# Kernel optimization log

Measured on AMD Instinct MI355X. Metric: run time of the kernel, lower is better.

The kernel has to match this reference:

```python
import jax, jax.numpy as jnp
import numpy as np

MEMORY_SIZE = 8192
FEATURE_DIM = 512
NUM_QUERIES = 32768
EPS = 1e-12  # guard for sqrt in cdist


def setup_inputs() -> dict:
    key = jax.random.key(0)
    k1, k2, k3, k4 = jax.random.split(key, 4)
    return {
        "features": jax.random.normal(k1, (MEMORY_SIZE, FEATURE_DIM), dtype=jnp.float32),
        "positions": jax.random.normal(k2, (MEMORY_SIZE, 3), dtype=jnp.float32),
        "query_positions": jax.random.normal(k3, (NUM_QUERIES, 3), dtype=jnp.float32),
        "position_embeddings": jax.random.normal(k4, (MEMORY_SIZE, 3), dtype=jnp.float32),
    }


def _cdist(a, b):
    # Euclidean distance via ||a||^2 + ||b||^2 - 2 a.b; avoids [Q,M,3] intermediate.
    a2 = jnp.sum(a * a, axis=-1, keepdims=True)          # [Q,1]
    b2 = jnp.sum(b * b, axis=-1, keepdims=True).T        # [1,M]
    d2 = a2 + b2 - 2.0 * (a @ b.T)                       # [Q,M]
    return jnp.sqrt(jnp.maximum(d2, EPS))


def reference(features, positions, query_positions, position_embeddings):
    # --- update ---
    positions_norm = positions / jnp.linalg.norm(positions, axis=-1, keepdims=True)
    embeddings_norm = position_embeddings / jnp.linalg.norm(position_embeddings, axis=-1, keepdims=True)
    sim = positions_norm @ embeddings_norm.T             # [M,M]
    attn = jax.nn.softmax(sim, axis=-1)
    memory = attn @ features                              # [M,F]
    new_pos_emb = attn @ positions                        # [M,3]
    # --- query ---
    dist = _cdist(query_positions, new_pos_emb)           # [Q,M]
    qattn = jax.nn.softmax(-dist, axis=-1)
    retrieved = qattn @ memory                            # [Q,F]
    return retrieved
```

## Files before the change

kernel.cpp:

```cpp
#include <hip/hip_runtime.h>
#include <stdint.h>
#include <stddef.h>

#define M_SZ 8192
#define F_DIM 512
#define N_Q 32768

typedef __attribute__((ext_vector_type(4))) float f32x4;
typedef __attribute__((ext_vector_type(8))) __bf16 bf16x8;
typedef __attribute__((ext_vector_type(2))) __bf16 bf16x2;

__device__ __forceinline__ float bits_to_f(unsigned u) {
    union { unsigned u; float f; } v; v.u = u; return v.f;
}
__device__ __forceinline__ unsigned pk_bf16(float a, float b) {
    union { bf16x2 v; unsigned u; } cv;
    cv.v.x = (__bf16)a; cv.v.y = (__bf16)b;
    return cv.u;
}
__device__ __forceinline__ unsigned short f2bf(float x) {
    union { bf16x2 v; unsigned u; } cv;
    cv.v.x = (__bf16)x; cv.v.y = (__bf16)0.0f;
    return (unsigned short)(cv.u & 0xffffu);
}
__device__ __forceinline__ bf16x8 as_bf16x8(uint4 u) {
    union { uint4 a; bf16x8 b; } cv; cv.a = u; return cv.b;
}

__global__ void prep_kernel(const float* __restrict__ pos,
                            const float* __restrict__ emb,
                            float* __restrict__ pn4,
                            float* __restrict__ en4,
                            float* __restrict__ pos4) {
    int i = blockIdx.x * 256 + threadIdx.x;
    if (i >= M_SZ) return;
    float x = pos[i * 3 + 0], y = pos[i * 3 + 1], z = pos[i * 3 + 2];
    float inv = 1.0f / __builtin_amdgcn_sqrtf(x * x + y * y + z * z);
    pn4[i * 4 + 0] = x * inv; pn4[i * 4 + 1] = y * inv;
    pn4[i * 4 + 2] = z * inv; pn4[i * 4 + 3] = 0.0f;
    pos4[i * 4 + 0] = x; pos4[i * 4 + 1] = y;
    pos4[i * 4 + 2] = z; pos4[i * 4 + 3] = 0.0f;
    float ex = emb[i * 3 + 0], ey = emb[i * 3 + 1], ez = emb[i * 3 + 2];
    float einv = 1.0f / __builtin_amdgcn_sqrtf(ex * ex + ey * ey + ez * ez);
    en4[i * 4 + 0] = ex * einv; en4[i * 4 + 1] = ey * einv;
    en4[i * 4 + 2] = ez * einv; en4[i * 4 + 3] = 0.0f;
}

__global__ void transpose_kernel(const float* __restrict__ feat,
                                 unsigned short* __restrict__ featT) {
    __shared__ float tile[64 * 65];
    const int jb = blockIdx.x * 64, fb = blockIdx.y * 64;
    const int t = threadIdx.x;
#pragma unroll
    for (int p = 0; p < 16; ++p) {
        int idx = p * 256 + t;
        int j = idx >> 6, f = idx & 63;
        tile[j * 65 + f] = feat[(size_t)(jb + j) * F_DIM + fb + f];
    }
    __syncthreads();
#pragma unroll
    for (int p = 0; p < 16; ++p) {
        int idx = p * 256 + t;
        int f = idx >> 6, j = idx & 63;
        featT[(size_t)(fb + f) * M_SZ + jb + j] = f2bf(tile[j * 65 + f]);
    }
}

__launch_bounds__(512, 2)
__global__ void build_memory_kernel(const float* __restrict__ pn4,
                                    const float* __restrict__ en4,
                                    const float* __restrict__ pos4,
                                    const unsigned short* __restrict__ featT,
                                    unsigned short* __restrict__ memT,
                                    float* __restrict__ npe4) {
    constexpr int BM = 32, BK = 32, PSTR = BK + 8;
    __shared__ unsigned short pbuf[2][BM * PSTR];
    __shared__ f32x4 red4[512];
    __shared__ float lbuf[BM];

    const int t = threadIdx.x;
    const int lane = t & 63, wv = t >> 6;
    const int col = lane & 15, quad = lane >> 4;
    const int mb = blockIdx.x * BM;
    const int r = t & 31, jq = t >> 5;

    const f32x4 pnr = ((const f32x4*)pn4)[mb + r];
    const f32x4* en = (const f32x4*)en4;
    const f32x4* ps = (const f32x4*)pos4;

    const unsigned short* bp[4];
#pragma unroll
    for (int n = 0; n < 4; ++n)
        bp[n] = featT + (size_t)(wv * 64 + n * 16 + col) * M_SZ + quad * 8;

    f32x4 acc[2][4];
    const f32x4 zero4 = {0.f, 0.f, 0.f, 0.f};
#pragma unroll
    for (int m = 0; m < 2; ++m)
#pragma unroll
        for (int n = 0; n < 4; ++n) acc[m][n] = zero4;
    float nx = 0.f, ny = 0.f, nz = 0.f, lp = 0.f;

    uint4 vbA[4], vbB[4];
#pragma unroll
    for (int n = 0; n < 4; ++n) vbA[n] = *(const uint4*)(bp[n]);

#define B_GEN_P(JB, SIDE)                                                    \
    {                                                                        \
        int j = (JB) + jq * 2;                                               \
        f32x4 e0 = en[j], e1 = en[j + 1];                                    \
        f32x4 p0 = ps[j], p1 = ps[j + 1];                                    \
        float s0 = fmaf(pnr.x, e0.x, fmaf(pnr.y, e0.y, pnr.z * e0.z));       \
        float s1 = fmaf(pnr.x, e1.x, fmaf(pnr.y, e1.y, pnr.z * e1.z));       \
        float w0 = __builtin_amdgcn_exp2f(s0 * 1.44269504f);                 \
        float w1 = __builtin_amdgcn_exp2f(s1 * 1.44269504f);                 \
        unsigned u = pk_bf16(w0, w1);                                        \
        float w0r = bits_to_f(u << 16), w1r = bits_to_f(u & 0xffff0000u);    \
        lp += w0r + w1r;                                                     \
        nx = fmaf(w0r, p0.x, fmaf(w1r, p1.x, nx));                           \
        ny = fmaf(w0r, p0.y, fmaf(w1r, p1.y, ny));                           \
        nz = fmaf(w0r, p0.z, fmaf(w1r, p1.z, nz));                           \
        *(unsigned*)(&pbuf[SIDE][r * PSTR + jq * 2]) = u;                    \
    }

#define B_MFMA(VB, SIDE)                                                     \
    {                                                                        \
        _Pragma("unroll") for (int m = 0; m < 2; ++m) {                      \
            bf16x8 a = *(const bf16x8*)(&pbuf[SIDE][(m * 16 + col) * PSTR + quad * 8]); \
            _Pragma("unroll") for (int n = 0; n < 4; ++n)                    \
                acc[m][n] = __builtin_amdgcn_mfma_f32_16x16x32_bf16(         \
                    a, as_bf16x8(VB[n]), acc[m][n], 0, 0, 0);                \
        }                                                                    \
    }

#define B_BODY(CUR, NXT, SIDE, JNXT)                                         \
    {                                                                        \
        _Pragma("unroll") for (int n = 0; n < 4; ++n) {                      \
            NXT[n] = *(const uint4*)(bp[n] + BK);                            \
            bp[n] += BK;                                                     \
        }                                                                    \
        B_GEN_P(JNXT, SIDE ^ 1)                                              \
        B_MFMA(CUR, SIDE)                                                    \
        __syncthreads();                                                     \
    }

    B_GEN_P(0, 0)
    __syncthreads();

    int jn = BK;
    for (int kt = 0; kt < 254; kt += 2) {
        B_BODY(vbA, vbB, 0, jn) jn += BK;
        B_BODY(vbB, vbA, 1, jn) jn += BK;
    }
    B_BODY(vbA, vbB, 0, jn)
    B_MFMA(vbB, 1)
#undef B_BODY
#undef B_MFMA
#undef B_GEN_P

    f32x4 mine = {nx, ny, nz, lp};
    red4[t] = mine;
    __syncthreads();
    if (t < BM) {
        f32x4 s = red4[t];
#pragma unroll
        for (int g = 1; g < 16; ++g) {
            f32x4 o = red4[t + 32 * g];
            s.x += o.x; s.y += o.y; s.z += o.z; s.w += o.w;
        }
        lbuf[t] = s.w;
        float inv = 1.0f / s.w;
        float X = s.x * inv, Y = s.y * inv, Z = s.z * inv;
        f32x4 o = {X, Y, Z, X * X + Y * Y + Z * Z};
        ((f32x4*)npe4)[mb + t] = o;
    }
    __syncthreads();

#pragma unroll
    for (int m = 0; m < 2; ++m) {
        f32x4 l4 = *(const f32x4*)(lbuf + m * 16 + quad * 4);
        f32x4 inv4 = {1.0f / l4.x, 1.0f / l4.y, 1.0f / l4.z, 1.0f / l4.w};
        int mg = mb + m * 16 + quad * 4;
#pragma unroll
        for (int n = 0; n < 4; ++n) {
            int fg = wv * 64 + n * 16 + col;
            uint2 o;
            o.x = pk_bf16(acc[m][n].x * inv4.x, acc[m][n].y * inv4.y);
            o.y = pk_bf16(acc[m][n].z * inv4.z, acc[m][n].w * inv4.w);
            *(uint2*)(memT + (size_t)fg * M_SZ + mg) = o;
        }
    }
}

__launch_bounds__(512, 2)
__global__ void query_kernel(const float* __restrict__ qpos,
                             const float* __restrict__ npe4,
                             const unsigned short* __restrict__ memT,
                             float* __restrict__ out) {
    constexpr int BM = 128, BK = 32, PSTR = BK + 8;
    __shared__ unsigned short pbuf[2][BM * PSTR];
    __shared__ float redl[512];
    __shared__ float lbuf[BM];

    const int t = threadIdx.x;
    const int lane = t & 63, wv = t >> 6;
    const int col = lane & 15, quad = lane >> 4;
    const int qb = blockIdx.x * BM;
    const int r = t & 127, jq = t >> 7;

    const float qx = qpos[(size_t)(qb + r) * 3 + 0];
    const float qy = qpos[(size_t)(qb + r) * 3 + 1];
    const float qz = qpos[(size_t)(qb + r) * 3 + 2];
    const float q2 = qx * qx + qy * qy + qz * qz;
    const float m2x = -2.0f * qx, m2y = -2.0f * qy, m2z = -2.0f * qz;

    const f32x4* nsrc = (const f32x4*)npe4;

    const unsigned short* bp[4];
#pragma unroll
    for (int n = 0; n < 4; ++n)
        bp[n] = memT + (size_t)(wv * 64 + n * 16 + col) * M_SZ + quad * 8;

    f32x4 acc[8][4];
    const f32x4 zero4 = {0.f, 0.f, 0.f, 0.f};
#pragma unroll
    for (int m = 0; m < 8; ++m)
#pragma unroll
        for (int n = 0; n < 4; ++n) acc[m][n] = zero4;
    float lp = 0.f;

    uint4 vbA[4], vbB[4];
#pragma unroll
    for (int n = 0; n < 4; ++n) vbA[n] = *(const uint4*)(bp[n]);

#define Q_GEN_P(JB, SIDE)                                                    \
    {                                                                        \
        unsigned pk4[4];                                                     \
        _Pragma("unroll") for (int i = 0; i < 8; i += 2) {                   \
            int j = (JB) + jq * 8 + i;                                       \
            f32x4 n0 = nsrc[j], n1 = nsrc[j + 1];                            \
            float s0 = fmaf(m2x, n0.x, fmaf(m2y, n0.y, fmaf(m2z, n0.z, q2 + n0.w))); \
            float s1 = fmaf(m2x, n1.x, fmaf(m2y, n1.y, fmaf(m2z, n1.z, q2 + n1.w))); \
            s0 = fmaxf(s0, 1e-12f); s1 = fmaxf(s1, 1e-12f);                  \
            float w0 = __builtin_amdgcn_exp2f(__builtin_amdgcn_sqrtf(s0) * -1.44269504f); \
            float w1 = __builtin_amdgcn_exp2f(__builtin_amdgcn_sqrtf(s1) * -1.44269504f); \
            unsigned u = pk_bf16(w0, w1);                                    \
            lp += bits_to_f(u << 16) + bits_to_f(u & 0xffff0000u);           \
            pk4[i >> 1] = u;                                                 \
        }                                                                    \
        *(uint4*)(&pbuf[SIDE][r * PSTR + jq * 8]) =                          \
            make_uint4(pk4[0], pk4[1], pk4[2], pk4[3]);                      \
    }

#define Q_MFMA(VB, SIDE)                                                     \
    {                                                                        \
        _Pragma("unroll") for (int m = 0; m < 8; ++m) {                      \
            bf16x8 a = *(const bf16x8*)(&pbuf[SIDE][(m * 16 + col) * PSTR + quad * 8]); \
            _Pragma("unroll") for (int n = 0; n < 4; ++n)                    \
                acc[m][n] = __builtin_amdgcn_mfma_f32_16x16x32_bf16(         \
                    a, as_bf16x8(VB[n]), acc[m][n], 0, 0, 0);                \
        }                                                                    \
    }

#define Q_BODY(CUR, NXT, SIDE, JNXT)                                         \
    {                                                                        \
        _Pragma("unroll") for (int n = 0; n < 4; ++n) {                      \
            NXT[n] = *(const uint4*)(bp[n] + BK);                            \
            bp[n] += BK;                                                     \
        }                                                                    \
        Q_GEN_P(JNXT, SIDE ^ 1)                                              \
        Q_MFMA(CUR, SIDE)                                                    \
        __syncthreads();                                                     \
    }

    Q_GEN_P(0, 0)
    __syncthreads();

    int jn = BK;
    for (int kt = 0; kt < 254; kt += 2) {
        Q_BODY(vbA, vbB, 0, jn) jn += BK;
        Q_BODY(vbB, vbA, 1, jn) jn += BK;
    }
    Q_BODY(vbA, vbB, 0, jn)
    Q_MFMA(vbB, 1)
#undef Q_BODY
#undef Q_MFMA
#undef Q_GEN_P

    redl[t] = lp;
    __syncthreads();
    if (t < BM) lbuf[t] = redl[t] + redl[t + 128] + redl[t + 256] + redl[t + 384];
    __syncthreads();

#pragma unroll
    for (int m = 0; m < 8; ++m) {
        f32x4 l4 = *(const f32x4*)(lbuf + m * 16 + quad * 4);
        f32x4 inv4 = {1.0f / l4.x, 1.0f / l4.y, 1.0f / l4.z, 1.0f / l4.w};
        int qg = qb + m * 16 + quad * 4;
#pragma unroll
        for (int n = 0; n < 4; ++n) {
            int fg = wv * 64 + n * 16 + col;
            out[(size_t)(qg + 0) * F_DIM + fg] = acc[m][n].x * inv4.x;
            out[(size_t)(qg + 1) * F_DIM + fg] = acc[m][n].y * inv4.y;
            out[(size_t)(qg + 2) * F_DIM + fg] = acc[m][n].z * inv4.z;
            out[(size_t)(qg + 3) * F_DIM + fg] = acc[m][n].w * inv4.w;
        }
    }
}

extern "C" void kernel_launch(void* const* d_in, const int* in_sizes, int n_in,
                              void* d_out, int out_size, void* d_ws, size_t ws_size,
                              hipStream_t stream) {
    const float* features  = (const float*)d_in[0];
    const float* positions = (const float*)d_in[1];
    const float* qpos      = (const float*)d_in[2];
    const float* pemb      = (const float*)d_in[3];
    float* out = (float*)d_out;
    char* ws = (char*)d_ws;

    unsigned short* featT = (unsigned short*)(ws);
    unsigned short* memT  = (unsigned short*)(ws + 8388608);
    float* npe4 = (float*)(ws + 16777216);
    float* pn4  = (float*)(ws + 16908288);
    float* en4  = (float*)(ws + 17039360);
    float* pos4 = (float*)(ws + 17170432);

    hipLaunchKernelGGL(prep_kernel, dim3(M_SZ / 256), dim3(256), 0, stream,
                       positions, pemb, pn4, en4, pos4);
    hipLaunchKernelGGL(transpose_kernel, dim3(M_SZ / 64, F_DIM / 64), dim3(256), 0, stream,
                       features, featT);
    hipLaunchKernelGGL(build_memory_kernel, dim3(M_SZ / 32), dim3(512), 0, stream,
                       pn4, en4, pos4, featT, memT, npe4);
    hipLaunchKernelGGL(query_kernel, dim3(N_Q / 128), dim3(512), 0, stream,
                       qpos, npe4, memT, out);
}
```

Baseline: 815.3 us.

## Deepen K-tiles in build kernel and split query kernel across feature halves

```diff
diff --git a/kernel.cpp b/kernel.cpp
--- a/kernel.cpp
+++ b/kernel.cpp
@@ -73,7 +73,7 @@
                                     const unsigned short* __restrict__ featT,
                                     unsigned short* __restrict__ memT,
                                     float* __restrict__ npe4) {
-    constexpr int BM = 32, BK = 32, PSTR = BK + 8;
+    constexpr int BM = 32, BK = 128, PSTR = BK + 8;
     __shared__ unsigned short pbuf[2][BM * PSTR];
     __shared__ f32x4 red4[512];
     __shared__ float lbuf[BM];
@@ -101,44 +101,55 @@
         for (int n = 0; n < 4; ++n) acc[m][n] = zero4;
     float nx = 0.f, ny = 0.f, nz = 0.f, lp = 0.f;
 
-    uint4 vbA[4], vbB[4];
-#pragma unroll
-    for (int n = 0; n < 4; ++n) vbA[n] = *(const uint4*)(bp[n]);
+    uint4 vbA[4][4], vbB[4][4];
+#pragma unroll
+    for (int ks = 0; ks < 4; ++ks)
+#pragma unroll
+        for (int n = 0; n < 4; ++n)
+            vbA[ks][n] = *(const uint4*)(bp[n] + ks * 32);
 
 #define B_GEN_P(JB, SIDE)                                                    \
     {                                                                        \
-        int j = (JB) + jq * 2;                                               \
-        f32x4 e0 = en[j], e1 = en[j + 1];                                    \
-        f32x4 p0 = ps[j], p1 = ps[j + 1];                                    \
-        float s0 = fmaf(pnr.x, e0.x, fmaf(pnr.y, e0.y, pnr.z * e0.z));       \
-        float s1 = fmaf(pnr.x, e1.x, fmaf(pnr.y, e1.y, pnr.z * e1.z));       \
-        float w0 = __builtin_amdgcn_exp2f(s0 * 1.44269504f);                 \
-        float w1 = __builtin_amdgcn_exp2f(s1 * 1.44269504f);                 \
-        unsigned u = pk_bf16(w0, w1);                                        \
-        float w0r = bits_to_f(u << 16), w1r = bits_to_f(u & 0xffff0000u);    \
-        lp += w0r + w1r;                                                     \
-        nx = fmaf(w0r, p0.x, fmaf(w1r, p1.x, nx));                           \
-        ny = fmaf(w0r, p0.y, fmaf(w1r, p1.y, ny));                           \
-        nz = fmaf(w0r, p0.z, fmaf(w1r, p1.z, nz));                           \
-        *(unsigned*)(&pbuf[SIDE][r * PSTR + jq * 2]) = u;                    \
+        unsigned pk4[4];                                                     \
+        _Pragma("unroll") for (int i = 0; i < 8; i += 2) {                   \
+            int j = (JB) + jq * 8 + i;                                       \
+            f32x4 e0 = en[j], e1 = en[j + 1];                                \
+            f32x4 p0 = ps[j], p1 = ps[j + 1];                                \
+            float s0 = fmaf(pnr.x, e0.x, fmaf(pnr.y, e0.y, pnr.z * e0.z));   \
+            float s1 = fmaf(pnr.x, e1.x, fmaf(pnr.y, e1.y, pnr.z * e1.z));   \
+            float w0 = __builtin_amdgcn_exp2f(s0 * 1.44269504f);             \
+            float w1 = __builtin_amdgcn_exp2f(s1 * 1.44269504f);             \
+            unsigned u = pk_bf16(w0, w1);                                    \
+            float w0r = bits_to_f(u << 16), w1r = bits_to_f(u & 0xffff0000u);\
+            lp += w0r + w1r;                                                 \
+            nx = fmaf(w0r, p0.x, fmaf(w1r, p1.x, nx));                       \
+            ny = fmaf(w0r, p0.y, fmaf(w1r, p1.y, ny));                       \
+            nz = fmaf(w0r, p0.z, fmaf(w1r, p1.z, nz));                       \
+            pk4[i >> 1] = u;                                                 \
+        }                                                                    \
+        *(uint4*)(&pbuf[SIDE][r * PSTR + jq * 8]) =                          \
+            make_uint4(pk4[0], pk4[1], pk4[2], pk4[3]);                      \
     }
 
 #define B_MFMA(VB, SIDE)                                                     \
     {                                                                        \
-        _Pragma("unroll") for (int m = 0; m < 2; ++m) {                      \
-            bf16x8 a = *(const bf16x8*)(&pbuf[SIDE][(m * 16 + col) * PSTR + quad * 8]); \
+        _Pragma("unroll") for (int ks = 0; ks < 4; ++ks) {                   \
+            _Pragma("unroll") for (int m = 0; m < 2; ++m) {                  \
+                bf16x8 a = *(const bf16x8*)(                                 \
+                    &pbuf[SIDE][(m * 16 + col) * PSTR + ks * 32 + quad * 8]);\
+                _Pragma("unroll") for (int n = 0; n < 4; ++n)                \
+                    acc[m][n] = __builtin_amdgcn_mfma_f32_16x16x32_bf16(     \
+                        a, as_bf16x8(VB[ks][n]), acc[m][n], 0, 0, 0);        \
+            }                                                                \
+        }                                                                    \
+    }
+
+#define B_BODY(CUR, NXT, SIDE, JNXT)                                         \
+    {                                                                        \
+        _Pragma("unroll") for (int ks = 0; ks < 4; ++ks)                     \
             _Pragma("unroll") for (int n = 0; n < 4; ++n)                    \
-                acc[m][n] = __builtin_amdgcn_mfma_f32_16x16x32_bf16(         \
-                    a, as_bf16x8(VB[n]), acc[m][n], 0, 0, 0);                \
-        }                                                                    \
-    }
-
-#define B_BODY(CUR, NXT, SIDE, JNXT)                                         \
-    {                                                                        \
-        _Pragma("unroll") for (int n = 0; n < 4; ++n) {                      \
-            NXT[n] = *(const uint4*)(bp[n] + BK);                            \
-            bp[n] += BK;                                                     \
-        }                                                                    \
+                NXT[ks][n] = *(const uint4*)(bp[n] + BK + ks * 32);          \
+        _Pragma("unroll") for (int n = 0; n < 4; ++n) bp[n] += BK;           \
         B_GEN_P(JNXT, SIDE ^ 1)                                              \
         B_MFMA(CUR, SIDE)                                                    \
         __syncthreads();                                                     \
@@ -148,7 +159,7 @@
     __syncthreads();
 
     int jn = BK;
-    for (int kt = 0; kt < 254; kt += 2) {
+    for (int kt = 0; kt < 62; kt += 2) {
         B_BODY(vbA, vbB, 0, jn) jn += BK;
         B_BODY(vbB, vbA, 1, jn) jn += BK;
     }
@@ -192,21 +203,21 @@
     }
 }
 
-__launch_bounds__(512, 2)
+__launch_bounds__(256, 2)
 __global__ void query_kernel(const float* __restrict__ qpos,
                              const float* __restrict__ npe4,
                              const unsigned short* __restrict__ memT,
                              float* __restrict__ out) {
-    constexpr int BM = 128, BK = 32, PSTR = BK + 8;
+    constexpr int BM = 64, BK = 64, PSTR = BK + 8;
     __shared__ unsigned short pbuf[2][BM * PSTR];
-    __shared__ float redl[512];
+    __shared__ float redl[256];
     __shared__ float lbuf[BM];
 
     const int t = threadIdx.x;
     const int lane = t & 63, wv = t >> 6;
     const int col = lane & 15, quad = lane >> 4;
-    const int qb = blockIdx.x * BM;
-    const int r = t & 127, jq = t >> 7;
+    const int qb = blockIdx.x * BM, fb = blockIdx.y * 256;
+    const int r = t & 63, jq = t >> 6;
 
     const float qx = qpos[(size_t)(qb + r) * 3 + 0];
     const float qy = qpos[(size_t)(qb + r) * 3 + 1];
@@ -219,25 +230,28 @@
     const unsigned short* bp[4];
 #pragma unroll
     for (int n = 0; n < 4; ++n)
-        bp[n] = memT + (size_t)(wv * 64 + n * 16 + col) * M_SZ + quad * 8;
-
-    f32x4 acc[8][4];
+        bp[n] = memT + (size_t)(fb + wv * 64 + n * 16 + col) * M_SZ + quad * 8;
+
+    f32x4 acc[4][4];
     const f32x4 zero4 = {0.f, 0.f, 0.f, 0.f};
 #pragma unroll
-    for (int m = 0; m < 8; ++m)
+    for (int m = 0; m < 4; ++m)
 #pragma unroll
         for (int n = 0; n < 4; ++n) acc[m][n] = zero4;
     float lp = 0.f;
 
-    uint4 vbA[4], vbB[4];
-#pragma unroll
-    for (int n = 0; n < 4; ++n) vbA[n] = *(const uint4*)(bp[n]);
+    uint4 vbA[2][4], vbB[2][4];
+#pragma unroll
+    for (int ks = 0; ks < 2; ++ks)
+#pragma unroll
+        for (int n = 0; n < 4; ++n)
+            vbA[ks][n] = *(const uint4*)(bp[n] + ks * 32);
 
 #define Q_GEN_P(JB, SIDE)                                                    \
     {                                                                        \
-        unsigned pk4[4];                                                     \
-        _Pragma("unroll") for (int i = 0; i < 8; i += 2) {                   \
-            int j = (JB) + jq * 8 + i;                                       \
+        unsigned pk8[8];                                                     \
+        _Pragma("unroll") for (int i = 0; i < 16; i += 2) {                  \
+            int j = (JB) + jq * 16 + i;                                      \
             f32x4 n0 = nsrc[j], n1 = nsrc[j + 1];                            \
             float s0 = fmaf(m2x, n0.x, fmaf(m2y, n0.y, fmaf(m2z, n0.z, q2 + n0.w))); \
             float s1 = fmaf(m2x, n1.x, fmaf(m2y, n1.y, fmaf(m2z, n1.z, q2 + n1.w))); \
@@ -246,28 +260,32 @@
             float w1 = __builtin_amdgcn_exp2f(__builtin_amdgcn_sqrtf(s1) * -1.44269504f); \
             unsigned u = pk_bf16(w0, w1);                                    \
             lp += bits_to_f(u << 16) + bits_to_f(u & 0xffff0000u);           \
-            pk4[i >> 1] = u;                                                 \
+            pk8[i >> 1] = u;                                                 \
         }                                                                    \
-        *(uint4*)(&pbuf[SIDE][r * PSTR + jq * 8]) =                          \
-            make_uint4(pk4[0], pk4[1], pk4[2], pk4[3]);                      \
+        uint4* pd = (uint4*)(&pbuf[SIDE][r * PSTR + jq * 16]);               \
+        pd[0] = make_uint4(pk8[0], pk8[1], pk8[2], pk8[3]);                  \
+        pd[1] = make_uint4(pk8[4], pk8[5], pk8[6], pk8[7]);                  \
     }
 
 #define Q_MFMA(VB, SIDE)                                                     \
     {                                                                        \
-        _Pragma("unroll") for (int m = 0; m < 8; ++m) {                      \
-            bf16x8 a = *(const bf16x8*)(&pbuf[SIDE][(m * 16 + col) * PSTR + quad * 8]); \
+        _Pragma("unroll") for (int ks = 0; ks < 2; ++ks) {                   \
+            _Pragma("unroll") for (int m = 0; m < 4; ++m) {                  \
+                bf16x8 a = *(const bf16x8*)(                                 \
+                    &pbuf[SIDE][(m * 16 + col) * PSTR + ks * 32 + quad * 8]);\
+                _Pragma("unroll") for (int n = 0; n < 4; ++n)                \
+                    acc[m][n] = __builtin_amdgcn_mfma_f32_16x16x32_bf16(     \
+                        a, as_bf16x8(VB[ks][n]), acc[m][n], 0, 0, 0);        \
+            }                                                                \
+        }                                                                    \
+    }
+
+#define Q_BODY(CUR, NXT, SIDE, JNXT)                                         \
+    {                                                                        \
+        _Pragma("unroll") for (int ks = 0; ks < 2; ++ks)                     \
             _Pragma("unroll") for (int n = 0; n < 4; ++n)                    \
-                acc[m][n] = __builtin_amdgcn_mfma_f32_16x16x32_bf16(         \
-                    a, as_bf16x8(VB[n]), acc[m][n], 0, 0, 0);                \
-        }                                                                    \
-    }
-
-#define Q_BODY(CUR, NXT, SIDE, JNXT)                                         \
-    {                                                                        \
-        _Pragma("unroll") for (int n = 0; n < 4; ++n) {                      \
-            NXT[n] = *(const uint4*)(bp[n] + BK);                            \
-            bp[n] += BK;                                                     \
-        }                                                                    \
+                NXT[ks][n] = *(const uint4*)(bp[n] + BK + ks * 32);          \
+        _Pragma("unroll") for (int n = 0; n < 4; ++n) bp[n] += BK;           \
         Q_GEN_P(JNXT, SIDE ^ 1)                                              \
         Q_MFMA(CUR, SIDE)                                                    \
         __syncthreads();                                                     \
@@ -277,7 +295,7 @@
     __syncthreads();
 
     int jn = BK;
-    for (int kt = 0; kt < 254; kt += 2) {
+    for (int kt = 0; kt < 126; kt += 2) {
         Q_BODY(vbA, vbB, 0, jn) jn += BK;
         Q_BODY(vbB, vbA, 1, jn) jn += BK;
     }
@@ -289,17 +307,17 @@
 
     redl[t] = lp;
     __syncthreads();
-    if (t < BM) lbuf[t] = redl[t] + redl[t + 128] + redl[t + 256] + redl[t + 384];
-    __syncthreads();
-
-#pragma unroll
-    for (int m = 0; m < 8; ++m) {
+    if (t < BM) lbuf[t] = redl[t] + redl[t + 64] + redl[t + 128] + redl[t + 192];
+    __syncthreads();
+
+#pragma unroll
+    for (int m = 0; m < 4; ++m) {
         f32x4 l4 = *(const f32x4*)(lbuf + m * 16 + quad * 4);
         f32x4 inv4 = {1.0f / l4.x, 1.0f / l4.y, 1.0f / l4.z, 1.0f / l4.w};
         int qg = qb + m * 16 + quad * 4;
 #pragma unroll
         for (int n = 0; n < 4; ++n) {
-            int fg = wv * 64 + n * 16 + col;
+            int fg = fb + wv * 64 + n * 16 + col;
             out[(size_t)(qg + 0) * F_DIM + fg] = acc[m][n].x * inv4.x;
             out[(size_t)(qg + 1) * F_DIM + fg] = acc[m][n].y * inv4.y;
             out[(size_t)(qg + 2) * F_DIM + fg] = acc[m][n].z * inv4.z;
@@ -331,6 +349,6 @@
                        features, featT);
     hipLaunchKernelGGL(build_memory_kernel, dim3(M_SZ / 32), dim3(512), 0, stream,
                        pn4, en4, pos4, featT, memT, npe4);
-    hipLaunchKernelGGL(query_kernel, dim3(N_Q / 128), dim3(512), 0, stream,
+    hipLaunchKernelGGL(query_kernel, dim3(N_Q / 64, 2), dim3(256), 0, stream,
                        qpos, npe4, memT, out);
 }
```

New measurement: 1.309 ms. +60.6%, slower.

## Shrink tiles and split feature dim to raise occupancy in build and query kernels

Applied to the files above, without the earlier changes.

```diff
diff --git a/kernel.cpp b/kernel.cpp
--- a/kernel.cpp
+++ b/kernel.cpp
@@ -66,32 +66,33 @@
     }
 }
 
-__launch_bounds__(512, 2)
+__launch_bounds__(256, 4)
 __global__ void build_memory_kernel(const float* __restrict__ pn4,
                                     const float* __restrict__ en4,
                                     const float* __restrict__ pos4,
                                     const unsigned short* __restrict__ featT,
                                     unsigned short* __restrict__ memT,
                                     float* __restrict__ npe4) {
-    constexpr int BM = 32, BK = 32, PSTR = BK + 8;
+    constexpr int BM = 32, BK = 32, PSTR = 40;
     __shared__ unsigned short pbuf[2][BM * PSTR];
-    __shared__ f32x4 red4[512];
+    __shared__ f32x4 red4[256];
     __shared__ float lbuf[BM];
 
     const int t = threadIdx.x;
     const int lane = t & 63, wv = t >> 6;
     const int col = lane & 15, quad = lane >> 4;
-    const int mb = blockIdx.x * BM;
+    const int mb = blockIdx.x * BM, fb = blockIdx.y * 256;
+    const bool y0 = (blockIdx.y == 0);
     const int r = t & 31, jq = t >> 5;
 
     const f32x4 pnr = ((const f32x4*)pn4)[mb + r];
     const f32x4* en = (const f32x4*)en4;
     const f32x4* ps = (const f32x4*)pos4;
 
-    const unsigned short* bp[4];
-#pragma unroll
-    for (int n = 0; n < 4; ++n)
-        bp[n] = featT + (size_t)(wv * 64 + n * 16 + col) * M_SZ + quad * 8;
+    const unsigned short* bp0 = featT + (size_t)(fb + wv * 64 + 0 + col) * M_SZ + quad * 8;
+    const unsigned short* bp1 = featT + (size_t)(fb + wv * 64 + 16 + col) * M_SZ + quad * 8;
+    const unsigned short* bp2 = featT + (size_t)(fb + wv * 64 + 32 + col) * M_SZ + quad * 8;
+    const unsigned short* bp3 = featT + (size_t)(fb + wv * 64 + 48 + col) * M_SZ + quad * 8;
 
     f32x4 acc[2][4];
     const f32x4 zero4 = {0.f, 0.f, 0.f, 0.f};
@@ -101,62 +102,59 @@
         for (int n = 0; n < 4; ++n) acc[m][n] = zero4;
     float nx = 0.f, ny = 0.f, nz = 0.f, lp = 0.f;
 
-    uint4 vbA[4], vbB[4];
-#pragma unroll
-    for (int n = 0; n < 4; ++n) vbA[n] = *(const uint4*)(bp[n]);
-
-#define B_GEN_P(JB, SIDE)                                                    \
+#define B_GEN(JB, SIDE)                                                      \
     {                                                                        \
-        int j = (JB) + jq * 2;                                               \
-        f32x4 e0 = en[j], e1 = en[j + 1];                                    \
-        f32x4 p0 = ps[j], p1 = ps[j + 1];                                    \
+        int j = (JB) + jq * 4;                                               \
+        f32x4 e0 = en[j], e1 = en[j + 1], e2 = en[j + 2], e3 = en[j + 3];    \
         float s0 = fmaf(pnr.x, e0.x, fmaf(pnr.y, e0.y, pnr.z * e0.z));       \
         float s1 = fmaf(pnr.x, e1.x, fmaf(pnr.y, e1.y, pnr.z * e1.z));       \
-        float w0 = __builtin_amdgcn_exp2f(s0 * 1.44269504f);                 \
-        float w1 = __builtin_amdgcn_exp2f(s1 * 1.44269504f);                 \
-        unsigned u = pk_bf16(w0, w1);                                        \
-        float w0r = bits_to_f(u << 16), w1r = bits_to_f(u & 0xffff0000u);    \
-        lp += w0r + w1r;                                                     \
-        nx = fmaf(w0r, p0.x, fmaf(w1r, p1.x, nx));                           \
-        ny = fmaf(w0r, p0.y, fmaf(w1r, p1.y, ny));                           \
-        nz = fmaf(w0r, p0.z, fmaf(w1r, p1.z, nz));                           \
-        *(unsigned*)(&pbuf[SIDE][r * PSTR + jq * 2]) = u;                    \
-    }
-
-#define B_MFMA(VB, SIDE)                                                     \
+        float s2 = fmaf(pnr.x, e2.x, fmaf(pnr.y, e2.y, pnr.z * e2.z));       \
+        float s3 = fmaf(pnr.x, e3.x, fmaf(pnr.y, e3.y, pnr.z * e3.z));       \
+        unsigned u0 = pk_bf16(__builtin_amdgcn_exp2f(s0 * 1.44269504f),      \
+                              __builtin_amdgcn_exp2f(s1 * 1.44269504f));     \
+        unsigned u1 = pk_bf16(__builtin_amdgcn_exp2f(s2 * 1.44269504f),      \
+                              __builtin_amdgcn_exp2f(s3 * 1.44269504f));     \
+        float w0 = bits_to_f(u0 << 16), w1 = bits_to_f(u0 & 0xffff0000u);    \
+        float w2 = bits_to_f(u1 << 16), w3 = bits_to_f(u1 & 0xffff0000u);    \
+        lp += (w0 + w1) + (w2 + w3);                                         \
+        if (y0) {                                                            \
+            f32x4 p0 = ps[j], p1 = ps[j + 1], p2 = ps[j + 2], p3 = ps[j + 3];\
+            nx += fmaf(w0, p0.x, w1 * p1.x) + fmaf(w2, p2.x, w3 * p3.x);     \
+            ny += fmaf(w0, p0.y, w1 * p1.y) + fmaf(w2, p2.y, w3 * p3.y);     \
+            nz += fmaf(w0, p0.z, w1 * p1.z) + fmaf(w2, p2.z, w3 * p3.z);     \
+        }                                                                    \
+        *(uint2*)(&pbuf[SIDE][r * PSTR + jq * 4]) = make_uint2(u0, u1);      \
+    }
+
+#define B_STEP(SIDE, DOGEN, DOSYNC, JB)                                      \
     {                                                                        \
+        uint4 vb0 = *(const uint4*)bp0; bp0 += BK;                           \
+        uint4 vb1 = *(const uint4*)bp1; bp1 += BK;                           \
+        uint4 vb2 = *(const uint4*)bp2; bp2 += BK;                           \
+        uint4 vb3 = *(const uint4*)bp3; bp3 += BK;                           \
+        if (DOGEN) B_GEN(JB, (SIDE) ^ 1)                                     \
         _Pragma("unroll") for (int m = 0; m < 2; ++m) {                      \
             bf16x8 a = *(const bf16x8*)(&pbuf[SIDE][(m * 16 + col) * PSTR + quad * 8]); \
-            _Pragma("unroll") for (int n = 0; n < 4; ++n)                    \
-                acc[m][n] = __builtin_amdgcn_mfma_f32_16x16x32_bf16(         \
-                    a, as_bf16x8(VB[n]), acc[m][n], 0, 0, 0);                \
+            acc[m][0] = __builtin_amdgcn_mfma_f32_16x16x32_bf16(a, as_bf16x8(vb0), acc[m][0], 0, 0, 0); \
+            acc[m][1] = __builtin_amdgcn_mfma_f32_16x16x32_bf16(a, as_bf16x8(vb1), acc[m][1], 0, 0, 0); \
+            acc[m][2] = __builtin_amdgcn_mfma_f32_16x16x32_bf16(a, as_bf16x8(vb2), acc[m][2], 0, 0, 0); \
+            acc[m][3] = __builtin_amdgcn_mfma_f32_16x16x32_bf16(a, as_bf16x8(vb3), acc[m][3], 0, 0, 0); \
         }                                                                    \
-    }
-
-#define B_BODY(CUR, NXT, SIDE, JNXT)                                         \
-    {                                                                        \
-        _Pragma("unroll") for (int n = 0; n < 4; ++n) {                      \
-            NXT[n] = *(const uint4*)(bp[n] + BK);                            \
-            bp[n] += BK;                                                     \
-        }                                                                    \
-        B_GEN_P(JNXT, SIDE ^ 1)                                              \
-        B_MFMA(CUR, SIDE)                                                    \
-        __syncthreads();                                                     \
-    }
-
-    B_GEN_P(0, 0)
+        if (DOSYNC) __syncthreads();                                         \
+    }
+
+    B_GEN(0, 0)
     __syncthreads();
 
     int jn = BK;
-    for (int kt = 0; kt < 254; kt += 2) {
-        B_BODY(vbA, vbB, 0, jn) jn += BK;
-        B_BODY(vbB, vbA, 1, jn) jn += BK;
-    }
-    B_BODY(vbA, vbB, 0, jn)
-    B_MFMA(vbB, 1)
-#undef B_BODY
-#undef B_MFMA
-#undef B_GEN_P
+    for (int i2 = 0; i2 < 127; ++i2) {
+        B_STEP(0, true, true, jn) jn += BK;
+        B_STEP(1, true, true, jn) jn += BK;
+    }
+    B_STEP(0, true, true, jn)
+    B_STEP(1, false, false, 0)
+#undef B_STEP
+#undef B_GEN
 
     f32x4 mine = {nx, ny, nz, lp};
     red4[t] = mine;
@@ -164,15 +162,17 @@
     if (t < BM) {
         f32x4 s = red4[t];
 #pragma unroll
-        for (int g = 1; g < 16; ++g) {
+        for (int g = 1; g < 8; ++g) {
             f32x4 o = red4[t + 32 * g];
             s.x += o.x; s.y += o.y; s.z += o.z; s.w += o.w;
         }
         lbuf[t] = s.w;
-        float inv = 1.0f / s.w;
-        float X = s.x * inv, Y = s.y * inv, Z = s.z * inv;
-        f32x4 o = {X, Y, Z, X * X + Y * Y + Z * Z};
-        ((f32x4*)npe4)[mb + t] = o;
+        if (y0) {
+            float inv = 1.0f / s.w;
+            float X = s.x * inv, Y = s.y * inv, Z = s.z * inv;
+            f32x4 o = {X, Y, Z, X * X + Y * Y + Z * Z};
+            ((f32x4*)npe4)[mb + t] = o;
+        }
     }
     __syncthreads();
 
@@ -183,7 +183,7 @@
         int mg = mb + m * 16 + quad * 4;
 #pragma unroll
         for (int n = 0; n < 4; ++n) {
-            int fg = wv * 64 + n * 16 + col;
+            int fg = fb + wv * 64 + n * 16 + col;
             uint2 o;
             o.x = pk_bf16(acc[m][n].x * inv4.x, acc[m][n].y * inv4.y);
             o.y = pk_bf16(acc[m][n].z * inv4.z, acc[m][n].w * inv4.w);
@@ -192,12 +192,12 @@
     }
 }
 
-__launch_bounds__(512, 2)
+__launch_bounds__(512, 4)
 __global__ void query_kernel(const float* __restrict__ qpos,
                              const float* __restrict__ npe4,
                              const unsigned short* __restrict__ memT,
                              float* __restrict__ out) {
-    constexpr int BM = 128, BK = 32, PSTR = BK + 8;
+    constexpr int BM = 64, BK = 32, PSTR = 40;
     __shared__ unsigned short pbuf[2][BM * PSTR];
     __shared__ float redl[512];
     __shared__ float lbuf[BM];
@@ -206,7 +206,7 @@
     const int lane = t & 63, wv = t >> 6;
     const int col = lane & 15, quad = lane >> 4;
     const int qb = blockIdx.x * BM;
-    const int r = t & 127, jq = t >> 7;
+    const int r = t & 63, jq = t >> 6;
 
     const float qx = qpos[(size_t)(qb + r) * 3 + 0];
     const float qy = qpos[(size_t)(qb + r) * 3 + 1];
@@ -216,84 +216,82 @@
 
     const f32x4* nsrc = (const f32x4*)npe4;
 
-    const unsigned short* bp[4];
-#pragma unroll
-    for (int n = 0; n < 4; ++n)
-        bp[n] = memT + (size_t)(wv * 64 + n * 16 + col) * M_SZ + quad * 8;
-
-    f32x4 acc[8][4];
+    const unsigned short* bp0 = memT + (size_t)(wv * 64 + 0 + col) * M_SZ + quad * 8;
+    const unsigned short* bp1 = memT + (size_t)(wv * 64 + 16 + col) * M_SZ + quad * 8;
+    const unsigned short* bp2 = memT + (size_t)(wv * 64 + 32 + col) * M_SZ + quad * 8;
+    const unsigned short* bp3 = memT + (size_t)(wv * 64 + 48 + col) * M_SZ + quad * 8;
+
+    f32x4 acc[4][4];
     const f32x4 zero4 = {0.f, 0.f, 0.f, 0.f};
 #pragma unroll
-    for (int m = 0; m < 8; ++m)
+    for (int m = 0; m < 4; ++m)
 #pragma unroll
         for (int n = 0; n < 4; ++n) acc[m][n] = zero4;
     float lp = 0.f;
 
-    uint4 vbA[4], vbB[4];
-#pragma unroll
-    for (int n = 0; n < 4; ++n) vbA[n] = *(const uint4*)(bp[n]);
-
-#define Q_GEN_P(JB, SIDE)                                                    \
+#define Q_GEN(JB, SIDE)                                                      \
     {                                                                        \
-        unsigned pk4[4];                                                     \
-        _Pragma("unroll") for (int i = 0; i < 8; i += 2) {                   \
-            int j = (JB) + jq * 8 + i;                                       \
-            f32x4 n0 = nsrc[j], n1 = nsrc[j + 1];                            \
-            float s0 = fmaf(m2x, n0.x, fmaf(m2y, n0.y, fmaf(m2z, n0.z, q2 + n0.w))); \
-            float s1 = fmaf(m2x, n1.x, fmaf(m2y, n1.y, fmaf(m2z, n1.z, q2 + n1.w))); \
-            s0 = fmaxf(s0, 1e-12f); s1 = fmaxf(s1, 1e-12f);                  \
-            float w0 = __builtin_amdgcn_exp2f(__builtin_amdgcn_sqrtf(s0) * -1.44269504f); \
-            float w1 = __builtin_amdgcn_exp2f(__builtin_amdgcn_sqrtf(s1) * -1.44269504f); \
-            unsigned u = pk_bf16(w0, w1);                                    \
-            lp += bits_to_f(u << 16) + bits_to_f(u & 0xffff0000u);           \
-            pk4[i >> 1] = u;                                                 \
+        int j = (JB) + jq * 4;                                               \
+        f32x4 n0 = nsrc[j], n1 = nsrc[j + 1], n2 = nsrc[j + 2], n3 = nsrc[j + 3]; \
+        float s0 = fmaf(m2x, n0.x, fmaf(m2y, n0.y, fmaf(m2z, n0.z, q2 + n0.w))); \
+        float s1 = fmaf(m2x, n1.x, fmaf(m2y, n1.y, fmaf(m2z, n1.z, q2 + n1.w))); \
+        float s2 = fmaf(m2x, n2.x, fmaf(m2y, n2.y, fmaf(m2z, n2.z, q2 + n2.w))); \
+        float s3 = fmaf(m2x, n3.x, fmaf(m2y, n3.y, fmaf(m2z, n3.z, q2 + n3.w))); \
+        s0 = fmaxf(s0, 1e-12f); s1 = fmaxf(s1, 1e-12f);                      \
+        s2 = fmaxf(s2, 1e-12f); s3 = fmaxf(s3, 1e-12f);                      \
+        float w0 = __builtin_amdgcn_exp2f(__builtin_amdgcn_sqrtf(s0) * -1.44269504f); \
+        float w1 = __builtin_amdgcn_exp2f(__builtin_amdgcn_sqrtf(s1) * -1.44269504f); \
+        float w2 = __builtin_amdgcn_exp2f(__builtin_amdgcn_sqrtf(s2) * -1.44269504f); \
+        float w3 = __builtin_amdgcn_exp2f(__builtin_amdgcn_sqrtf(s3) * -1.44269504f); \
+        unsigned u0 = pk_bf16(w0, w1);                                       \
+        unsigned u1 = pk_bf16(w2, w3);                                       \
+        lp += (bits_to_f(u0 << 16) + bits_to_f(u0 & 0xffff0000u)) +          \
+              (bits_to_f(u1 << 16) + bits_to_f(u1 & 0xffff0000u));           \
+        *(uint2*)(&pbuf[SIDE][r * PSTR + jq * 4]) = make_uint2(u0, u1);      \
+    }
+
+#define Q_STEP(SIDE, DOGEN, DOSYNC, JB)                                      \
+    {                                                                        \
+        uint4 vb0 = *(const uint4*)bp0; bp0 += BK;                           \
+        uint4 vb1 = *(const uint4*)bp1; bp1 += BK;                           \
+        uint4 vb2 = *(const uint4*)bp2; bp2 += BK;                           \
+        uint4 vb3 = *(const uint4*)bp3; bp3 += BK;                           \
+        if (DOGEN) Q_GEN(JB, (SIDE) ^ 1)                                     \
+        _Pragma("unroll") for (int m = 0; m < 4; ++m) {                      \
+            bf16x8 a = *(const bf16x8*)(&pbuf[SIDE][(m * 16 + col) * PSTR + quad * 8]); \
+            acc[m][0] = __builtin_amdgcn_mfma_f32_16x16x32_bf16(a, as_bf16x8(vb0), acc[m][0], 0, 0, 0); \
+            acc[m][1] = __builtin_amdgcn_mfma_f32_16x16x32_bf16(a, as_bf16x8(vb1), acc[m][1], 0, 0, 0); \
+            acc[m][2] = __builtin_amdgcn_mfma_f32_16x16x32_bf16(a, as_bf16x8(vb2), acc[m][2], 0, 0, 0); \
+            acc[m][3] = __builtin_amdgcn_mfma_f32_16x16x32_bf16(a, as_bf16x8(vb3), acc[m][3], 0, 0, 0); \
         }                                                                    \
-        *(uint4*)(&pbuf[SIDE][r * PSTR + jq * 8]) =                          \
-            make_uint4(pk4[0], pk4[1], pk4[2], pk4[3]);                      \
-    }
-
-#define Q_MFMA(VB, SIDE)                                                     \
-    {                                                                        \
-        _Pragma("unroll") for (int m = 0; m < 8; ++m) {                      \
-            bf16x8 a = *(const bf16x8*)(&pbuf[SIDE][(m * 16 + col) * PSTR + quad * 8]); \
-            _Pragma("unroll") for (int n = 0; n < 4; ++n)                    \
-                acc[m][n] = __builtin_amdgcn_mfma_f32_16x16x32_bf16(         \
-                    a, as_bf16x8(VB[n]), acc[m][n], 0, 0, 0);                \
-        }                                                                    \
-    }
-
-#define Q_BODY(CUR, NXT, SIDE, JNXT)                                         \
-    {                                                                        \
-        _Pragma("unroll") for (int n = 0; n < 4; ++n) {                      \
-            NXT[n] = *(const uint4*)(bp[n] + BK);                            \
-            bp[n] += BK;                                                     \
-        }                                                                    \
-        Q_GEN_P(JNXT, SIDE ^ 1)                                              \
-        Q_MFMA(CUR, SIDE)                                                    \
-        __syncthreads();                                                     \
-    }
-
-    Q_GEN_P(0, 0)
+        if (DOSYNC) __syncthreads();                                         \
+    }
+
+    Q_GEN(0, 0)
     __syncthreads();
 
     int jn = BK;
-    for (int kt = 0; kt < 254; kt += 2) {
-        Q_BODY(vbA, vbB, 0, jn) jn += BK;
-        Q_BODY(vbB, vbA, 1, jn) jn += BK;
-    }
-    Q_BODY(vbA, vbB, 0, jn)
-    Q_MFMA(vbB, 1)
-#undef Q_BODY
-#undef Q_MFMA
-#undef Q_GEN_P
+    for (int i2 = 0; i2 < 127; ++i2) {
+        Q_STEP(0, true, true, jn) jn += BK;
+        Q_STEP(1, true, true, jn) jn += BK;
+    }
+    Q_STEP(0, true, true, jn)
+    Q_STEP(1, false, false, 0)
+#undef Q_STEP
+#undef Q_GEN
 
     redl[t] = lp;
     __syncthreads();
-    if (t < BM) lbuf[t] = redl[t] + redl[t + 128] + redl[t + 256] + redl[t + 384];
-    __syncthreads();
-
-#pragma unroll
-    for (int m = 0; m < 8; ++m) {
+    if (t < BM) {
+        float s = redl[t];
+#pragma unroll
+        for (int g = 1; g < 8; ++g) s += redl[t + 64 * g];
+        lbuf[t] = s;
+    }
+    __syncthreads();
+
+#pragma unroll
+    for (int m = 0; m < 4; ++m) {
         f32x4 l4 = *(const f32x4*)(lbuf + m * 16 + quad * 4);
         f32x4 inv4 = {1.0f / l4.x, 1.0f / l4.y, 1.0f / l4.z, 1.0f / l4.w};
         int qg = qb + m * 16 + quad * 4;
@@ -329,8 +327,8 @@
                        positions, pemb, pn4, en4, pos4);
     hipLaunchKernelGGL(transpose_kernel, dim3(M_SZ / 64, F_DIM / 64), dim3(256), 0, stream,
                        features, featT);
-    hipLaunchKernelGGL(build_memory_kernel, dim3(M_SZ / 32), dim3(512), 0, stream,
+    hipLaunchKernelGGL(build_memory_kernel, dim3(M_SZ / 32, 2), dim3(256), 0, stream,
                        pn4, en4, pos4, featT, memT, npe4);
-    hipLaunchKernelGGL(query_kernel, dim3(N_Q / 128), dim3(512), 0, stream,
+    hipLaunchKernelGGL(query_kernel, dim3(N_Q / 64), dim3(512), 0, stream,
                        qpos, npe4, memT, out);
 }
```

Result: slower. 1.016 ms (+24.6%).
